# Performance work log

Hardware: AMD Instinct MI355X
Metric: run time of the kernel (lower is better)

Reference implementation:

```python
import jax, jax.numpy as jnp
from jax import lax
import numpy as np

INPUT_DIM = 64
AUX_DIM = 32
HIDDEN = [512, 512]
OUTPUT_DIM = 128
BATCH = 64
SEQ = 512


def _lstm_params(key, in_dim, hidden):
    # PyTorch nn.LSTM init: U(-1/sqrt(H), 1/sqrt(H)); gate order i,f,g,o
    k = 1.0 / np.sqrt(hidden)
    ks = jax.random.split(key, 4)
    W_ih = jax.random.uniform(ks[0], (4 * hidden, in_dim), jnp.float32, -k, k)
    W_hh = jax.random.uniform(ks[1], (4 * hidden, hidden), jnp.float32, -k, k)
    b_ih = jax.random.uniform(ks[2], (4 * hidden,), jnp.float32, -k, k)
    b_hh = jax.random.uniform(ks[3], (4 * hidden,), jnp.float32, -k, k)
    return W_ih, W_hh, b_ih, b_hh


def setup_inputs() -> dict:
    key = jax.random.key(0)
    k_x, k_aux, k_l0, k_l1, k_w, k_b = jax.random.split(key, 6)
    primary_input = jax.random.normal(k_x, (BATCH, SEQ, INPUT_DIM), jnp.float32)
    auxiliary_input = jax.random.normal(k_aux, (BATCH, AUX_DIM), jnp.float32)
    W_ih0, W_hh0, b_ih0, b_hh0 = _lstm_params(k_l0, INPUT_DIM + AUX_DIM, HIDDEN[0])
    W_ih1, W_hh1, b_ih1, b_hh1 = _lstm_params(k_l1, HIDDEN[0], HIDDEN[1])
    k_out = 1.0 / np.sqrt(HIDDEN[-1])
    W_out = jax.random.uniform(k_w, (OUTPUT_DIM, HIDDEN[-1]), jnp.float32, -k_out, k_out)
    b_out = jax.random.uniform(k_b, (OUTPUT_DIM,), jnp.float32, -k_out, k_out)
    return {
        "primary_input": primary_input, "auxiliary_input": auxiliary_input,
        "W_ih0": W_ih0, "W_hh0": W_hh0, "b_ih0": b_ih0, "b_hh0": b_hh0,
        "W_ih1": W_ih1, "W_hh1": W_hh1, "b_ih1": b_ih1, "b_hh1": b_hh1,
        "W_out": W_out, "b_out": b_out,
    }


def _lstm_layer(x, W_ih, W_hh, b_ih, b_hh):
    # x: [B, S, D] -> hidden sequence [B, S, H]; zero initial (h, c)
    B = x.shape[0]
    H = W_hh.shape[1]
    # Precompute input projection for all timesteps: [B, S, 4H]
    x_proj = jnp.einsum('bsd,gd->bsg', x, W_ih) + b_ih + b_hh

    def step(carry, xt):
        h, c = carry  # [B, H] each
        gates = xt + h @ W_hh.T  # [B, 4H]
        i, f, g, o = jnp.split(gates, 4, axis=-1)
        i = jax.nn.sigmoid(i)
        f = jax.nn.sigmoid(f)
        g = jnp.tanh(g)
        o = jax.nn.sigmoid(o)
        c = f * c + i * g
        h = o * jnp.tanh(c)
        return (h, c), h

    h0 = jnp.zeros((B, H), x.dtype)
    (_, _), hs = lax.scan(step, (h0, h0), jnp.swapaxes(x_proj, 0, 1))
    return jnp.swapaxes(hs, 0, 1)  # [B, S, H]


def reference(primary_input, auxiliary_input,
              W_ih0, W_hh0, b_ih0, b_hh0,
              W_ih1, W_hh1, b_ih1, b_hh1,
              W_out, b_out):
    S = primary_input.shape[1]
    aux = jnp.broadcast_to(auxiliary_input[:, None, :],
                           (auxiliary_input.shape[0], S, auxiliary_input.shape[1]))
    x = jnp.concatenate([primary_input, aux], axis=2)  # [B, S, input+aux]
    x = _lstm_layer(x, W_ih0, W_hh0, b_ih0, b_hh0)
    x = _lstm_layer(x, W_ih1, W_hh1, b_ih1, b_hh1)
    last = x[:, -1, :]  # [B, H]
    return last @ W_out.T + b_out  # [B, output_dim]
```

## Files before the change

### kernel.cpp

```cpp
#include <hip/hip_runtime.h>

#define BATCH 64
#define SEQ   512
#define HID   512
#define DPRIM 64
#define DAUX  32
#define CT    16
#define NCHUNK 32
#define NBAT  32
#define WP    520
#define XPI   104
#define PST   33

#define WS_HB0HI  0u
#define WS_HB0LO  131072u
#define WS_HB1HI  262144u
#define WS_HB1LO  393216u
#define WS_SLOT0  524288u
#define WS_SLOT1  526336u
#define WS_GDONE  528384u
#define WS_XPD    530432u
#define WS_STATE_END 532480u
#define WS_PHH0HI 532480u
#define WS_PHH0LO 2629632u
#define WS_PHH1HI 4726784u
#define WS_PHH1LO 6823936u
#define WS_PIH1HI 8921088u
#define WS_PIH1LO 11018240u
#define WS_PIH0HI 13115392u
#define WS_PIH0LO 13508608u
#define WS_BSUM0  13901824u
#define WS_BSUM1  13910016u
#define WS_WOT    13918208u
#define WS_HIST   14180352u
#define WS_XP0    18374656u
#define WS_XP1    26763264u

typedef short s16x8 __attribute__((ext_vector_type(8)));
typedef float f32x4 __attribute__((ext_vector_type(4)));
typedef unsigned long long u64t;
typedef unsigned int u32t;
typedef unsigned short u16t;

__device__ __forceinline__ float sigm(float x)  { return 1.f / (1.f + __expf(-x)); }
__device__ __forceinline__ float tanh_f(float x){ return 1.f - 2.f / (__expf(2.f * x) + 1.f); }
__device__ __forceinline__ u16t f2b(float f) {
    u32t u = __float_as_uint(f);
    u += 0x7fffu + ((u >> 16) & 1u);
    return (u16t)(u >> 16);
}
__device__ __forceinline__ void split2(float f, u16t* hi, u16t* lo) {
    u16t h = f2b(f);
    float r = f - __uint_as_float((u32t)h << 16);
    *hi = h; *lo = f2b(r);
}
__device__ __forceinline__ u64t ld_coh64(const u64t* p) {
    return __hip_atomic_load(p, __ATOMIC_RELAXED, __HIP_MEMORY_SCOPE_AGENT);
}
__device__ __forceinline__ float ld_cohf(const float* p) {
    return __hip_atomic_load(p, __ATOMIC_RELAXED, __HIP_MEMORY_SCOPE_AGENT);
}
__device__ __forceinline__ void st_coh32(u32t* p, u32t v) {
    __hip_atomic_store(p, v, __ATOMIC_RELAXED, __HIP_MEMORY_SCOPE_AGENT);
}
__device__ __forceinline__ void st_cohf(float* p, float v) {
    __hip_atomic_store(p, v, __ATOMIC_RELAXED, __HIP_MEMORY_SCOPE_AGENT);
}
__device__ __forceinline__ int ld_slot(const int* p) {
    return __hip_atomic_load(p, __ATOMIC_RELAXED, __HIP_MEMORY_SCOPE_AGENT);
}
__device__ __forceinline__ void st_slot(int* p, int v) {
    __hip_atomic_store(p, v, __ATOMIC_RELAXED, __HIP_MEMORY_SCOPE_AGENT);
}
#define MFMA16(a,b,c) __builtin_amdgcn_mfma_f32_16x16x32_bf16(a,b,c,0,0,0)

__device__ __forceinline__ void stage_w(const u16t* ph, const u16t* pl,
                                        u16t* dh, u16t* dl, int u0, int tid) {
    int rl = tid >> 4, j = tid & 15;
    int grow = (rl >> 3) * HID + u0 + (rl & 7);
    const u64t* sh = (const u64t*)(ph + (size_t)grow * HID);
    const u64t* sl = (const u64t*)(pl + (size_t)grow * HID);
    u64t* th = (u64t*)(dh + (size_t)rl * WP);
    u64t* tl2 = (u64t*)(dl + (size_t)rl * WP);
#pragma unroll
    for (int q = 0; q < 8; ++q) { int s = q * 16 + j; th[s] = sh[s]; tl2[s] = sl[s]; }
}

__global__ void prep_kernel(const float* __restrict__ Wih0, const float* __restrict__ Whh0,
                            const float* __restrict__ bih0, const float* __restrict__ bhh0,
                            const float* __restrict__ Wih1, const float* __restrict__ Whh1,
                            const float* __restrict__ bih1, const float* __restrict__ bhh1,
                            const float* __restrict__ Wout, char* __restrict__ ws)
{
    int idx = blockIdx.x * 256 + threadIdx.x;
    u16t h, l;
    split2(Whh0[idx], &h, &l);
    ((u16t*)(ws + WS_PHH0HI))[idx] = h; ((u16t*)(ws + WS_PHH0LO))[idx] = l;
    split2(Whh1[idx], &h, &l);
    ((u16t*)(ws + WS_PHH1HI))[idx] = h; ((u16t*)(ws + WS_PHH1LO))[idx] = l;
    split2(Wih1[idx], &h, &l);
    ((u16t*)(ws + WS_PIH1HI))[idx] = h; ((u16t*)(ws + WS_PIH1LO))[idx] = l;
    if (idx < 2048 * 96) {
        split2(Wih0[idx], &h, &l);
        ((u16t*)(ws + WS_PIH0HI))[idx] = h; ((u16t*)(ws + WS_PIH0LO))[idx] = l;
    }
    if (idx < 2048) {
        ((float*)(ws + WS_BSUM0))[idx] = bih0[idx] + bhh0[idx];
        ((float*)(ws + WS_BSUM1))[idx] = bih1[idx] + bhh1[idx];
    }
    if (idx < 65536) {
        ((float*)(ws + WS_WOT))[idx] = Wout[(size_t)(idx & 127) * HID + (idx >> 7)];
    }
}

__device__ __forceinline__ void do_step(
    int t, int c, int tl, int tid, int wid, int col, int kg,
    int b0, int u0, int ug,
    u16t* Whi, u16t* Wlo, u16t* Hhi, u16t* Hlo, float* Ps, float* Cs,
    u16t* hbhi, u16t* hblo, int* slots_self,
    const float* xp_self, bool coh_xq, u32t* hist_ring)
{
    const int p = t & 1;
    float xq0 = 0.f, xq1 = 0.f, xq2 = 0.f, xq3 = 0.f;
    if (tid < 256) {
        int b = tid >> 3, u = tid & 7;
        const float* xr = xp_self + (size_t)(b * CT + tl) * 32;
        if (coh_xq) {
            xq0 = ld_cohf(xr + u);      xq1 = ld_cohf(xr + 8 + u);
            xq2 = ld_cohf(xr + 16 + u); xq3 = ld_cohf(xr + 24 + u);
        } else {
            xq0 = xr[u]; xq1 = xr[8 + u]; xq2 = xr[16 + u]; xq3 = xr[24 + u];
        }
    }
    if (tid < 64) {
        while (true) {
            int v = ld_slot(slots_self + tid * 4);
            if (__all(v >= t)) break;
            __builtin_amdgcn_s_sleep(1);
        }
    }
    __syncthreads();
    {
        int b = tid >> 4, j = tid & 15;
        const u64t* sh = (const u64t*)(hbhi + (size_t)((p ^ 1) * BATCH + b0 + b) * HID);
        const u64t* sl = (const u64t*)(hblo + (size_t)((p ^ 1) * BATCH + b0 + b) * HID);
        u64t* th = (u64t*)(Hhi + (size_t)b * WP);
        u64t* tl2 = (u64t*)(Hlo + (size_t)b * WP);
#pragma unroll
        for (int q = 0; q < 8; ++q) {
            int s = q * 16 + j;
            u64t vh = ld_coh64(sh + s);
            u64t vl = ld_coh64(sl + s);
            th[s] = vh; tl2[s] = vl;
        }
    }
    __syncthreads();
    if (wid < 4) {
        int rt = wid >> 1, bt = wid & 1;
        const u16t* wah = Whi + (size_t)(rt * 16 + col) * WP;
        const u16t* wal = Wlo + (size_t)(rt * 16 + col) * WP;
        const u16t* hbh = Hhi + (size_t)(bt * 16 + col) * WP;
        const u16t* hbl = Hlo + (size_t)(bt * 16 + col) * WP;
        f32x4 a0 = {0.f, 0.f, 0.f, 0.f}, a1 = {0.f, 0.f, 0.f, 0.f};
#pragma unroll
        for (int k2 = 0; k2 < 8; ++k2) {
            int ko0 = k2 * 64 + kg * 8;
            int ko1 = ko0 + 32;
            s16x8 ah0 = *(const s16x8*)(wah + ko0), al0 = *(const s16x8*)(wal + ko0);
            s16x8 bh0 = *(const s16x8*)(hbh + ko0), bl0 = *(const s16x8*)(hbl + ko0);
            s16x8 ah1 = *(const s16x8*)(wah + ko1), al1 = *(const s16x8*)(wal + ko1);
            s16x8 bh1 = *(const s16x8*)(hbh + ko1), bl1 = *(const s16x8*)(hbl + ko1);
            a0 = MFMA16(ah0, bh0, a0); a1 = MFMA16(ah1, bh1, a1);
            a0 = MFMA16(ah0, bl0, a0); a1 = MFMA16(ah1, bl1, a1);
            a0 = MFMA16(al0, bh0, a0); a1 = MFMA16(al1, bh1, a1);
        }
        a0 = a0 + a1;
#pragma unroll
        for (int j = 0; j < 4; ++j)
            Ps[(rt * 16 + kg * 4 + j) * PST + bt * 16 + col] = a0[j];
    }
    __syncthreads();
    if (tid < 256) {
        int b = tid >> 3, u = tid & 7;
        float gi = Ps[(u)      * PST + b] + xq0;
        float gf = Ps[(8 + u)  * PST + b] + xq1;
        float gg = Ps[(16 + u) * PST + b] + xq2;
        float go = Ps[(24 + u) * PST + b] + xq3;
        float si = sigm(gi), sf = sigm(gf), so = sigm(go);
        float tg = tanh_f(gg);
        float cN = sf * Cs[tid] + si * tg;
        Cs[tid] = cN;
        float hN = so * tanh_f(cN);
        u16t hi, lo; split2(hN, &hi, &lo);
        int e = (b0 + b) * HID + u0 + u;
        int ph = __shfl_xor((int)hi, 1);
        int pl = __shfl_xor((int)lo, 1);
        if ((u & 1) == 0) {
            st_coh32((u32t*)hbhi + (size_t)p * (BATCH * HID / 2) + (e >> 1),
                     (u32t)hi | ((u32t)ph << 16));
            st_coh32((u32t*)hblo + (size_t)p * (BATCH * HID / 2) + (e >> 1),
                     (u32t)lo | ((u32t)pl << 16));
        }
        if (hist_ring) {
            st_coh32(hist_ring + ((size_t)((c & 1) * BATCH + b0 + b) * CT + tl) * HID + u0 + u,
                     ((u32t)hi << 16) | (u32t)lo);
        }
    }
    __syncthreads();
    if (tid == 0) st_slot(slots_self + ug * 4, t + 1);
}

__global__ __launch_bounds__(512, 2)
void mega_kernel(const float* __restrict__ prim, const float* __restrict__ aux,
                 char* __restrict__ ws)
{
    __shared__ __align__(16) unsigned char smem[151808];
    u16t* Whi  = (u16t*)smem;
    u16t* Wlo  = (u16t*)(smem + 33280);
    u16t* Hhi  = (u16t*)(smem + 66560);
    u16t* Hlo  = (u16t*)(smem + 99840);
    u16t* XWhi = (u16t*)(smem + 133120);
    u16t* XWlo = (u16t*)(smem + 139776);
    float* Ps  = (float*)(smem + 146432);
    float* Cs  = (float*)(smem + 150656);
    float* Bs  = (float*)(smem + 151680);

    const int tid  = threadIdx.x;
    const int wgid = blockIdx.x;
    const int layer = wgid >> 7;
    const int lwg  = wgid & 127;
    const int bg   = (lwg >> 2) & 1;
    const int ug   = ((lwg >> 3) << 2) | (lwg & 3);
    const int b0   = bg * NBAT;
    const int u0   = ug * 8;
    const int lane = tid & 63;
    const int wid  = tid >> 6;
    const int col  = lane & 15;
    const int kg   = lane >> 4;

    u16t* hbhi = (u16t*)(ws + (layer ? WS_HB1HI : WS_HB0HI));
    u16t* hblo = (u16t*)(ws + (layer ? WS_HB1LO : WS_HB0LO));
    int* slots_self = (int*)(ws + (layer ? WS_SLOT1 : WS_SLOT0)) + bg * 256;
    int* slots_l0   = (int*)(ws + WS_SLOT0) + bg * 256;
    int* gdone      = (int*)(ws + WS_GDONE) + bg * 256;
    int* xpd        = (int*)(ws + WS_XPD)   + bg * 256;
    const float* bsum = (const float*)(ws + (layer ? WS_BSUM1 : WS_BSUM0));
    u32t* hist = (u32t*)(ws + WS_HIST);
    float* xpregion = (float*)(ws + (layer ? WS_XP1 : WS_XP0));
    float* xp_self = xpregion + (size_t)lwg * 16384;

    if (tid < 256) Cs[tid] = 0.f;
    if (tid < 32) {
        int grow = (tid >> 3) * HID + u0 + (tid & 7);
        Bs[tid] = bsum[grow];
    }
    if (layer == 0) {
        stage_w((u16t*)(ws + WS_PHH0HI), (u16t*)(ws + WS_PHH0LO), Whi, Wlo, u0, tid);
        for (int s = tid; s < 32 * 24; s += 512) {
            int rl = s / 24, sl = s % 24;
            int grow = (rl >> 3) * HID + u0 + (rl & 7);
            u64t v  = *((const u64t*)((u16t*)(ws + WS_PIH0HI) + (size_t)grow * 96) + sl);
            u64t v2 = *((const u64t*)((u16t*)(ws + WS_PIH0LO) + (size_t)grow * 96) + sl);
            *((u64t*)(XWhi + (size_t)rl * XPI) + sl) = v;
            *((u64t*)(XWlo + (size_t)rl * XPI) + sl) = v2;
        }
    }
    __syncthreads();

    if (layer == 0) {
        for (int c = 0; c < NCHUNK; ++c) {
            {
                f32x4 acc[4][2];
#pragma unroll
                for (int m4 = 0; m4 < 4; ++m4)
#pragma unroll
                    for (int nt = 0; nt < 2; ++nt)
                        acc[m4][nt] = (f32x4){0.f, 0.f, 0.f, 0.f};
#pragma unroll
                for (int kt = 0; kt < 3; ++kt) {
                    int k0 = kt * 32 + kg * 8;
                    s16x8 ah0 = *(const s16x8*)(XWhi + (size_t)(col) * XPI + k0);
                    s16x8 al0 = *(const s16x8*)(XWlo + (size_t)(col) * XPI + k0);
                    s16x8 ah1 = *(const s16x8*)(XWhi + (size_t)(16 + col) * XPI + k0);
                    s16x8 al1 = *(const s16x8*)(XWlo + (size_t)(16 + col) * XPI + k0);
#pragma unroll
                    for (int m4 = 0; m4 < 4; ++m4) {
                        int bb = wid * 4 + m4;
                        float xv[8];
                        if (kt < 2) {
                            const float* pr = prim + ((size_t)(b0 + bb) * SEQ + c * CT + col) * DPRIM + k0;
                            float4 v0 = *(const float4*)pr;
                            float4 v1 = *(const float4*)(pr + 4);
                            xv[0] = v0.x; xv[1] = v0.y; xv[2] = v0.z; xv[3] = v0.w;
                            xv[4] = v1.x; xv[5] = v1.y; xv[6] = v1.z; xv[7] = v1.w;
                        } else {
                            const float* ax = aux + (size_t)(b0 + bb) * DAUX + kg * 8;
                            float4 v0 = *(const float4*)ax;
                            float4 v1 = *(const float4*)(ax + 4);
                            xv[0] = v0.x; xv[1] = v0.y; xv[2] = v0.z; xv[3] = v0.w;
                            xv[4] = v1.x; xv[5] = v1.y; xv[6] = v1.z; xv[7] = v1.w;
                        }
                        u16t hh[8], ll[8];
#pragma unroll
                        for (int j = 0; j < 8; ++j) split2(xv[j], &hh[j], &ll[j]);
                        s16x8 bh, bl;
#pragma unroll
                        for (int j = 0; j < 8; ++j) { bh[j] = (short)hh[j]; bl[j] = (short)ll[j]; }
                        acc[m4][0] = MFMA16(ah0, bh, acc[m4][0]);
                        acc[m4][0] = MFMA16(ah0, bl, acc[m4][0]);
                        acc[m4][0] = MFMA16(al0, bh, acc[m4][0]);
                        acc[m4][1] = MFMA16(ah1, bh, acc[m4][1]);
                        acc[m4][1] = MFMA16(ah1, bl, acc[m4][1]);
                        acc[m4][1] = MFMA16(al1, bh, acc[m4][1]);
                    }
                }
#pragma unroll
                for (int m4 = 0; m4 < 4; ++m4) {
                    int m = (wid * 4 + m4) * 16 + col;
#pragma unroll
                    for (int nt = 0; nt < 2; ++nt)
#pragma unroll
                        for (int j = 0; j < 4; ++j) {
                            int gr = nt * 16 + kg * 4 + j;
                            xp_self[(size_t)m * 32 + gr] = acc[m4][nt][j] + Bs[gr];
                        }
                }
            }
            if (c >= 2) {
                if (tid < 64) {
                    while (true) {
                        int v = ld_slot(gdone + tid * 4);
                        if (__all(v >= c - 1)) break;
                        __builtin_amdgcn_s_sleep(1);
                    }
                }
            }
            __syncthreads();
            for (int tl = 0; tl < CT; ++tl)
                do_step(c * CT + tl, c, tl, tid, wid, col, kg, b0, u0, ug,
                        Whi, Wlo, Hhi, Hlo, Ps, Cs, hbhi, hblo, slots_self,
                        xp_self, false, hist);
        }
    } else {
        u16t* Bthi = Whi;
        u16t* Btlo = Hhi;
        const int gm = ug >> 3, gn = ug & 7;
        for (int c = 0; c < NCHUNK; ++c) {
            if (tid < 64) {
                while (true) {
                    int v = ld_slot(slots_l0 + tid * 4);
                    if (__all(v >= (c + 1) * CT)) break;
                    __builtin_amdgcn_s_sleep(1);
                }
            }
            __syncthreads();
            {
                int i = tid >> 3, j = tid & 7;
                int m = gm * 64 + i;
                int gb = b0 + (m >> 4), tl2 = m & 15;
                const u64t* src = (const u64t*)(hist + ((size_t)((c & 1) * BATCH + gb) * CT + tl2) * HID);
                u64t* dh = (u64t*)(Bthi + (size_t)i * WP);
                u64t* dl = (u64t*)(Btlo + (size_t)i * WP);
#pragma unroll
                for (int q = 0; q < 16; ++q) {
                    int g = q * 8 + j;
                    u64t w0 = ld_coh64(src + g * 2);
                    u64t w1 = ld_coh64(src + g * 2 + 1);
                    u32t e0 = (u32t)w0, e1 = (u32t)(w0 >> 32);
                    u32t e2 = (u32t)w1, e3 = (u32t)(w1 >> 32);
                    dh[g] = (u64t)(e0 >> 16) | ((u64t)(e1 >> 16) << 16) |
                            ((u64t)(e2 >> 16) << 32) | ((u64t)(e3 >> 16) << 48);
                    dl[g] = (u64t)(e0 & 0xffffu) | ((u64t)(e1 & 0xffffu) << 16) |
                            ((u64t)(e2 & 0xffffu) << 32) | ((u64t)(e3 & 0xffffu) << 48);
                }
            }
            __syncthreads();
            if (tid == 0) st_slot(gdone + ug * 4, c + 1);
            {
                const u16t* pih = (const u16t*)(ws + WS_PIH1HI);
                const u16t* pil = (const u16t*)(ws + WS_PIH1LO);
                int Rb0 = gn * 256 + (wid * 2) * 16 + col;
                int Rb1 = Rb0 + 16;
                int g0 = ((Rb0 >> 3) & 3) * HID + (Rb0 >> 5) * 8 + (Rb0 & 7);
                int g1 = ((Rb1 >> 3) & 3) * HID + (Rb1 >> 5) * 8 + (Rb1 & 7);
                const u16t* a0h = pih + (size_t)g0 * HID;
                const u16t* a0l = pil + (size_t)g0 * HID;
                const u16t* a1h = pih + (size_t)g1 * HID;
                const u16t* a1l = pil + (size_t)g1 * HID;
                float biasv[2][4];
#pragma unroll
                for (int nt = 0; nt < 2; ++nt)
#pragma unroll
                    for (int j = 0; j < 4; ++j) {
                        int R = gn * 256 + (wid * 2 + nt) * 16 + kg * 4 + j;
                        biasv[nt][j] = bsum[((R >> 3) & 3) * HID + (R >> 5) * 8 + (R & 7)];
                    }
                f32x4 acc[4][2];
#pragma unroll
                for (int mt = 0; mt < 4; ++mt)
#pragma unroll
                    for (int nt = 0; nt < 2; ++nt)
                        acc[mt][nt] = (f32x4){0.f, 0.f, 0.f, 0.f};
                for (int kt = 0; kt < 16; ++kt) {
                    int k0 = kt * 32 + kg * 8;
                    s16x8 ah0 = *(const s16x8*)(a0h + k0), al0 = *(const s16x8*)(a0l + k0);
                    s16x8 ah1 = *(const s16x8*)(a1h + k0), al1 = *(const s16x8*)(a1l + k0);
#pragma unroll
                    for (int mt = 0; mt < 4; ++mt) {
                        const u16t* bth = Bthi + (size_t)(mt * 16 + col) * WP;
                        const u16t* btl = Btlo + (size_t)(mt * 16 + col) * WP;
                        s16x8 bh = *(const s16x8*)(bth + k0), bl = *(const s16x8*)(btl + k0);
                        acc[mt][0] = MFMA16(ah0, bh, acc[mt][0]);
                        acc[mt][0] = MFMA16(ah0, bl, acc[mt][0]);
                        acc[mt][0] = MFMA16(al0, bh, acc[mt][0]);
                        acc[mt][1] = MFMA16(ah1, bh, acc[mt][1]);
                        acc[mt][1] = MFMA16(ah1, bl, acc[mt][1]);
                        acc[mt][1] = MFMA16(al1, bh, acc[mt][1]);
                    }
                }
#pragma unroll
                for (int mt = 0; mt < 4; ++mt)
#pragma unroll
                    for (int nt = 0; nt < 2; ++nt)
#pragma unroll
                        for (int j = 0; j < 4; ++j) {
                            int m = gm * 64 + mt * 16 + col;
                            int R = gn * 256 + (wid * 2 + nt) * 16 + kg * 4 + j;
                            int ugt = R >> 5, rl = R & 31;
                            int lwgt = ((ugt >> 2) << 3) | (bg << 2) | (ugt & 3);
                            st_cohf(xpregion + (size_t)lwgt * 16384 + (size_t)m * 32 + rl,
                                    acc[mt][nt][j] + biasv[nt][j]);
                        }
            }
            __syncthreads();
            if (tid == 0) st_slot(xpd + ug * 4, c + 1);
            stage_w((u16t*)(ws + WS_PHH1HI), (u16t*)(ws + WS_PHH1LO), Whi, Wlo, u0, tid);
            if (tid < 64) {
                while (true) {
                    int v = ld_slot(xpd + tid * 4);
                    if (__all(v >= c + 1)) break;
                    __builtin_amdgcn_s_sleep(1);
                }
            }
            __syncthreads();
            for (int tl = 0; tl < CT; ++tl)
                do_step(c * CT + tl, c, tl, tid, wid, col, kg, b0, u0, ug,
                        Whi, Wlo, Hhi, Hlo, Ps, Cs, hbhi, hblo, slots_self,
                        xp_self, true, nullptr);
        }
    }
}

__global__ void outproj_kernel(const char* __restrict__ ws, const float* __restrict__ bout,
                               float* __restrict__ out)
{
    __shared__ float hs[HID];
    int b = blockIdx.x;
    const u16t* hh = (const u16t*)(ws + WS_HB1HI) + (size_t)(BATCH + b) * HID;
    const u16t* hl = (const u16t*)(ws + WS_HB1LO) + (size_t)(BATCH + b) * HID;
    for (int i = threadIdx.x; i < HID; i += 128)
        hs[i] = __uint_as_float((u32t)hh[i] << 16) + __uint_as_float((u32t)hl[i] << 16);
    __syncthreads();
    int o = threadIdx.x;
    const float* Wot = (const float*)(ws + WS_WOT);
    float acc = bout[o];
#pragma unroll 8
    for (int k = 0; k < HID; ++k) acc = fmaf(hs[k], Wot[k * 128 + o], acc);
    out[b * 128 + o] = acc;
}

extern "C" void kernel_launch(void* const* d_in, const int* in_sizes, int n_in,
                              void* d_out, int out_size, void* d_ws, size_t ws_size,
                              hipStream_t stream)
{
    (void)in_sizes; (void)n_in; (void)out_size; (void)ws_size;
    const float* prim = (const float*)d_in[0];
    const float* aux  = (const float*)d_in[1];
    const float* Wih0 = (const float*)d_in[2];
    const float* Whh0 = (const float*)d_in[3];
    const float* bih0 = (const float*)d_in[4];
    const float* bhh0 = (const float*)d_in[5];
    const float* Wih1 = (const float*)d_in[6];
    const float* Whh1 = (const float*)d_in[7];
    const float* bih1 = (const float*)d_in[8];
    const float* bhh1 = (const float*)d_in[9];
    const float* Wout = (const float*)d_in[10];
    const float* bout = (const float*)d_in[11];
    float* out = (float*)d_out;
    char* wsc  = (char*)d_ws;

    hipMemsetAsync(wsc, 0, WS_STATE_END, stream);
    prep_kernel<<<4096, 256, 0, stream>>>(Wih0, Whh0, bih0, bhh0,
                                          Wih1, Whh1, bih1, bhh1, Wout, wsc);

    void* margs[] = {(void*)&prim, (void*)&aux, (void*)&wsc};
    hipLaunchCooperativeKernel((void*)mega_kernel, dim3(256), dim3(512), margs, 0, stream);

    outproj_kernel<<<64, 128, 0, stream>>>(wsc, bout, out);
}
```

Before: 3.701 ms.

## Keep recurrent weights in registers and split K across all eight waves

The per-step recurrent matmul now uses all 8 waves, splitting K in half, instead of only 4. Each wave holds its W_hh fragments in registers for the whole chunk, and the previous hidden state is loaded straight from global memory into MFMA operands rather than staged through LDS. The aim is to cut two __syncthreads and the LDS staging from every serial timestep, and partial sums from the two K halves are added in the gate stage. Each wave now spin-waits only on the 32 slots it needs, and h and history stores are widened to 64-bit. The cost is higher register pressure and more polling traffic per wave.

```diff
diff --git a/kernel.cpp b/kernel.cpp
--- a/kernel.cpp
+++ b/kernel.cpp
@@ -38,6 +38,7 @@
 
 typedef short s16x8 __attribute__((ext_vector_type(8)));
 typedef float f32x4 __attribute__((ext_vector_type(4)));
+typedef unsigned long long u64x2 __attribute__((ext_vector_type(2)));
 typedef unsigned long long u64t;
 typedef unsigned int u32t;
 typedef unsigned short u16t;
@@ -54,13 +55,17 @@
     float r = f - __uint_as_float((u32t)h << 16);
     *hi = h; *lo = f2b(r);
 }
+__device__ __forceinline__ s16x8 mk_s16x8(u64t a, u64t b) {
+    u64x2 t; t.x = a; t.y = b;
+    return __builtin_bit_cast(s16x8, t);
+}
 __device__ __forceinline__ u64t ld_coh64(const u64t* p) {
     return __hip_atomic_load(p, __ATOMIC_RELAXED, __HIP_MEMORY_SCOPE_AGENT);
 }
 __device__ __forceinline__ float ld_cohf(const float* p) {
     return __hip_atomic_load(p, __ATOMIC_RELAXED, __HIP_MEMORY_SCOPE_AGENT);
 }
-__device__ __forceinline__ void st_coh32(u32t* p, u32t v) {
+__device__ __forceinline__ void st_coh64w(u64t* p, u64t v) {
     __hip_atomic_store(p, v, __ATOMIC_RELAXED, __HIP_MEMORY_SCOPE_AGENT);
 }
 __device__ __forceinline__ void st_cohf(float* p, float v) {
@@ -74,16 +79,19 @@
 }
 #define MFMA16(a,b,c) __builtin_amdgcn_mfma_f32_16x16x32_bf16(a,b,c,0,0,0)
 
-__device__ __forceinline__ void stage_w(const u16t* ph, const u16t* pl,
-                                        u16t* dh, u16t* dl, int u0, int tid) {
-    int rl = tid >> 4, j = tid & 15;
-    int grow = (rl >> 3) * HID + u0 + (rl & 7);
-    const u64t* sh = (const u64t*)(ph + (size_t)grow * HID);
-    const u64t* sl = (const u64t*)(pl + (size_t)grow * HID);
-    u64t* th = (u64t*)(dh + (size_t)rl * WP);
-    u64t* tl2 = (u64t*)(dl + (size_t)rl * WP);
-#pragma unroll
-    for (int q = 0; q < 8; ++q) { int s = q * 16 + j; th[s] = sh[s]; tl2[s] = sl[s]; }
+__device__ __forceinline__ void load_afrag(const u16t* ph, const u16t* pl,
+                                           int u0, int col, int kg, int rt, int kh,
+                                           s16x8* ah, s16x8* al) {
+    int r = rt * 16 + col;
+    int grow = (r >> 3) * HID + u0 + (r & 7);
+    const u16t* sh = ph + (size_t)grow * HID;
+    const u16t* sl = pl + (size_t)grow * HID;
+#pragma unroll
+    for (int k2 = 0; k2 < 8; ++k2) {
+        int ko = (kh * 8 + k2) * 32 + kg * 8;
+        ah[k2] = *(const s16x8*)(sh + ko);
+        al[k2] = *(const s16x8*)(sl + ko);
+    }
 }
 
 __global__ void prep_kernel(const float* __restrict__ Wih0, const float* __restrict__ Whh0,
@@ -114,9 +122,11 @@
 }
 
 __device__ __forceinline__ void do_step(
-    int t, int c, int tl, int tid, int wid, int col, int kg,
+    int t, int c, int tl, int tid, int col, int kg,
+    int rt, int bt, int kh,
     int b0, int u0, int ug,
-    u16t* Whi, u16t* Wlo, u16t* Hhi, u16t* Hlo, float* Ps, float* Cs,
+    const s16x8* ah, const s16x8* al,
+    float* Ps, float* Cs,
     u16t* hbhi, u16t* hblo, int* slots_self,
     const float* xp_self, bool coh_xq, u32t* hist_ring)
 {
@@ -132,78 +142,67 @@
             xq0 = xr[u]; xq1 = xr[8 + u]; xq2 = xr[16 + u]; xq3 = xr[24 + u];
         }
     }
-    if (tid < 64) {
+    {
+        int lane = tid & 63;
+        const int* sp = slots_self + (kh * 32 + (lane & 31)) * 4;
         while (true) {
-            int v = ld_slot(slots_self + tid * 4);
+            int v = (lane < 32) ? ld_slot(sp) : 0x7fffffff;
             if (__all(v >= t)) break;
             __builtin_amdgcn_s_sleep(1);
         }
     }
-    __syncthreads();
-    {
-        int b = tid >> 4, j = tid & 15;
-        const u64t* sh = (const u64t*)(hbhi + (size_t)((p ^ 1) * BATCH + b0 + b) * HID);
-        const u64t* sl = (const u64t*)(hblo + (size_t)((p ^ 1) * BATCH + b0 + b) * HID);
-        u64t* th = (u64t*)(Hhi + (size_t)b * WP);
-        u64t* tl2 = (u64t*)(Hlo + (size_t)b * WP);
-#pragma unroll
-        for (int q = 0; q < 8; ++q) {
-            int s = q * 16 + j;
-            u64t vh = ld_coh64(sh + s);
-            u64t vl = ld_coh64(sl + s);
-            th[s] = vh; tl2[s] = vl;
-        }
-    }
-    __syncthreads();
-    if (wid < 4) {
-        int rt = wid >> 1, bt = wid & 1;
-        const u16t* wah = Whi + (size_t)(rt * 16 + col) * WP;
-        const u16t* wal = Wlo + (size_t)(rt * 16 + col) * WP;
-        const u16t* hbh = Hhi + (size_t)(bt * 16 + col) * WP;
-        const u16t* hbl = Hlo + (size_t)(bt * 16 + col) * WP;
-        f32x4 a0 = {0.f, 0.f, 0.f, 0.f}, a1 = {0.f, 0.f, 0.f, 0.f};
-#pragma unroll
-        for (int k2 = 0; k2 < 8; ++k2) {
-            int ko0 = k2 * 64 + kg * 8;
-            int ko1 = ko0 + 32;
-            s16x8 ah0 = *(const s16x8*)(wah + ko0), al0 = *(const s16x8*)(wal + ko0);
-            s16x8 bh0 = *(const s16x8*)(hbh + ko0), bl0 = *(const s16x8*)(hbl + ko0);
-            s16x8 ah1 = *(const s16x8*)(wah + ko1), al1 = *(const s16x8*)(wal + ko1);
-            s16x8 bh1 = *(const s16x8*)(hbh + ko1), bl1 = *(const s16x8*)(hbl + ko1);
-            a0 = MFMA16(ah0, bh0, a0); a1 = MFMA16(ah1, bh1, a1);
-            a0 = MFMA16(ah0, bl0, a0); a1 = MFMA16(ah1, bl1, a1);
-            a0 = MFMA16(al0, bh0, a0); a1 = MFMA16(al1, bh1, a1);
-        }
-        a0 = a0 + a1;
-#pragma unroll
-        for (int j = 0; j < 4; ++j)
-            Ps[(rt * 16 + kg * 4 + j) * PST + bt * 16 + col] = a0[j];
-    }
+    asm volatile("" ::: "memory");
+    const size_t brow = (size_t)((p ^ 1) * BATCH + b0 + bt * 16 + col) * HID;
+    s16x8 bh[8], bl[8];
+#pragma unroll
+    for (int k2 = 0; k2 < 8; ++k2) {
+        int ko = (kh * 8 + k2) * 32 + kg * 8;
+        u64t h0 = ld_coh64((const u64t*)(hbhi + brow + ko));
+        u64t h1 = ld_coh64((const u64t*)(hbhi + brow + ko + 4));
+        u64t l0 = ld_coh64((const u64t*)(hblo + brow + ko));
+        u64t l1 = ld_coh64((const u64t*)(hblo + brow + ko + 4));
+        bh[k2] = mk_s16x8(h0, h1);
+        bl[k2] = mk_s16x8(l0, l1);
+    }
+    f32x4 a0 = {0.f, 0.f, 0.f, 0.f}, a1 = {0.f, 0.f, 0.f, 0.f};
+#pragma unroll
+    for (int k2 = 0; k2 < 8; ++k2) {
+        a0 = MFMA16(ah[k2], bh[k2], a0);
+        a1 = MFMA16(ah[k2], bl[k2], a1);
+        a0 = MFMA16(al[k2], bh[k2], a0);
+    }
+    a0 = a0 + a1;
+#pragma unroll
+    for (int j = 0; j < 4; ++j)
+        Ps[((kh << 5) + rt * 16 + kg * 4 + j) * PST + bt * 16 + col] = a0[j];
     __syncthreads();
     if (tid < 256) {
         int b = tid >> 3, u = tid & 7;
-        float gi = Ps[(u)      * PST + b] + xq0;
-        float gf = Ps[(8 + u)  * PST + b] + xq1;
-        float gg = Ps[(16 + u) * PST + b] + xq2;
-        float go = Ps[(24 + u) * PST + b] + xq3;
+        float gi = Ps[(u)      * PST + b] + Ps[(32 + u) * PST + b] + xq0;
+        float gf = Ps[(8 + u)  * PST + b] + Ps[(40 + u) * PST + b] + xq1;
+        float gg = Ps[(16 + u) * PST + b] + Ps[(48 + u) * PST + b] + xq2;
+        float go = Ps[(24 + u) * PST + b] + Ps[(56 + u) * PST + b] + xq3;
         float si = sigm(gi), sf = sigm(gf), so = sigm(go);
         float tg = tanh_f(gg);
         float cN = sf * Cs[tid] + si * tg;
         Cs[tid] = cN;
         float hN = so * tanh_f(cN);
         u16t hi, lo; split2(hN, &hi, &lo);
-        int e = (b0 + b) * HID + u0 + u;
-        int ph = __shfl_xor((int)hi, 1);
-        int pl = __shfl_xor((int)lo, 1);
-        if ((u & 1) == 0) {
-            st_coh32((u32t*)hbhi + (size_t)p * (BATCH * HID / 2) + (e >> 1),
-                     (u32t)hi | ((u32t)ph << 16));
-            st_coh32((u32t*)hblo + (size_t)p * (BATCH * HID / 2) + (e >> 1),
-                     (u32t)lo | ((u32t)pl << 16));
+        u32t wh = (u32t)hi | (((u32t)(u16t)__shfl_xor((int)hi, 1)) << 16);
+        u32t wl = (u32t)lo | (((u32t)(u16t)__shfl_xor((int)lo, 1)) << 16);
+        u64t qh = (u64t)wh | ((u64t)(u32t)__shfl_xor((int)wh, 2) << 32);
+        u64t ql = (u64t)wl | ((u64t)(u32t)__shfl_xor((int)wl, 2) << 32);
+        size_t e = ((size_t)p * BATCH + b0 + b) * HID + u0 + u;
+        if ((u & 3) == 0) {
+            st_coh64w((u64t*)hbhi + (e >> 2), qh);
+            st_coh64w((u64t*)hblo + (e >> 2), ql);
         }
         if (hist_ring) {
-            st_coh32(hist_ring + ((size_t)((c & 1) * BATCH + b0 + b) * CT + tl) * HID + u0 + u,
-                     ((u32t)hi << 16) | (u32t)lo);
+            u32t pk = ((u32t)hi << 16) | (u32t)lo;
+            u64t qp = (u64t)pk | ((u64t)(u32t)__shfl_xor((int)pk, 1) << 32);
+            if ((u & 1) == 0)
+                st_coh64w((u64t*)(hist_ring +
+                    ((size_t)((c & 1) * BATCH + b0 + b) * CT + tl) * HID + u0 + u), qp);
         }
     }
     __syncthreads();
@@ -214,16 +213,14 @@
 void mega_kernel(const float* __restrict__ prim, const float* __restrict__ aux,
                  char* __restrict__ ws)
 {
-    __shared__ __align__(16) unsigned char smem[151808];
-    u16t* Whi  = (u16t*)smem;
-    u16t* Wlo  = (u16t*)(smem + 33280);
-    u16t* Hhi  = (u16t*)(smem + 66560);
-    u16t* Hlo  = (u16t*)(smem + 99840);
+    __shared__ __align__(16) unsigned char smem[156032];
+    u16t* Bthi = (u16t*)smem;
+    u16t* Btlo = (u16t*)(smem + 66560);
     u16t* XWhi = (u16t*)(smem + 133120);
     u16t* XWlo = (u16t*)(smem + 139776);
     float* Ps  = (float*)(smem + 146432);
-    float* Cs  = (float*)(smem + 150656);
-    float* Bs  = (float*)(smem + 151680);
+    float* Cs  = (float*)(smem + 154880);
+    float* Bs  = (float*)(smem + 155904);
 
     const int tid  = threadIdx.x;
     const int wgid = blockIdx.x;
@@ -237,6 +234,9 @@
     const int wid  = tid >> 6;
     const int col  = lane & 15;
     const int kg   = lane >> 4;
+    const int rt   = (wid >> 1) & 1;
+    const int bt   = wid & 1;
+    const int kh   = wid >> 2;
 
     u16t* hbhi = (u16t*)(ws + (layer ? WS_HB1HI : WS_HB0HI));
     u16t* hblo = (u16t*)(ws + (layer ? WS_HB1LO : WS_HB0LO));
@@ -255,7 +255,6 @@
         Bs[tid] = bsum[grow];
     }
     if (layer == 0) {
-        stage_w((u16t*)(ws + WS_PHH0HI), (u16t*)(ws + WS_PHH0LO), Whi, Wlo, u0, tid);
         for (int s = tid; s < 32 * 24; s += 512) {
             int rl = s / 24, sl = s % 24;
             int grow = (rl >> 3) * HID + u0 + (rl & 7);
@@ -303,15 +302,15 @@
                         u16t hh[8], ll[8];
 #pragma unroll
                         for (int j = 0; j < 8; ++j) split2(xv[j], &hh[j], &ll[j]);
-                        s16x8 bh, bl;
-#pragma unroll
-                        for (int j = 0; j < 8; ++j) { bh[j] = (short)hh[j]; bl[j] = (short)ll[j]; }
-                        acc[m4][0] = MFMA16(ah0, bh, acc[m4][0]);
-                        acc[m4][0] = MFMA16(ah0, bl, acc[m4][0]);
-                        acc[m4][0] = MFMA16(al0, bh, acc[m4][0]);
-                        acc[m4][1] = MFMA16(ah1, bh, acc[m4][1]);
-                        acc[m4][1] = MFMA16(ah1, bl, acc[m4][1]);
-                        acc[m4][1] = MFMA16(al1, bh, acc[m4][1]);
+                        s16x8 bhv, blv;
+#pragma unroll
+                        for (int j = 0; j < 8; ++j) { bhv[j] = (short)hh[j]; blv[j] = (short)ll[j]; }
+                        acc[m4][0] = MFMA16(ah0, bhv, acc[m4][0]);
+                        acc[m4][0] = MFMA16(ah0, blv, acc[m4][0]);
+                        acc[m4][0] = MFMA16(al0, bhv, acc[m4][0]);
+                        acc[m4][1] = MFMA16(ah1, bhv, acc[m4][1]);
+                        acc[m4][1] = MFMA16(ah1, blv, acc[m4][1]);
+                        acc[m4][1] = MFMA16(al1, bhv, acc[m4][1]);
                     }
                 }
 #pragma unroll
@@ -326,6 +325,9 @@
                         }
                 }
             }
+            s16x8 ahf[8], alf[8];
+            load_afrag((const u16t*)(ws + WS_PHH0HI), (const u16t*)(ws + WS_PHH0LO),
+                       u0, col, kg, rt, kh, ahf, alf);
             if (c >= 2) {
                 if (tid < 64) {
                     while (true) {
@@ -337,13 +339,11 @@
             }
             __syncthreads();
             for (int tl = 0; tl < CT; ++tl)
-                do_step(c * CT + tl, c, tl, tid, wid, col, kg, b0, u0, ug,
-                        Whi, Wlo, Hhi, Hlo, Ps, Cs, hbhi, hblo, slots_self,
+                do_step(c * CT + tl, c, tl, tid, col, kg, rt, bt, kh, b0, u0, ug,
+                        ahf, alf, Ps, Cs, hbhi, hblo, slots_self,
                         xp_self, false, hist);
         }
     } else {
-        u16t* Bthi = Whi;
-        u16t* Btlo = Hhi;
         const int gm = ug >> 3, gn = ug & 7;
         for (int c = 0; c < NCHUNK; ++c) {
             if (tid < 64) {
@@ -409,13 +409,13 @@
                     for (int mt = 0; mt < 4; ++mt) {
                         const u16t* bth = Bthi + (size_t)(mt * 16 + col) * WP;
                         const u16t* btl = Btlo + (size_t)(mt * 16 + col) * WP;
-                        s16x8 bh = *(const s16x8*)(bth + k0), bl = *(const s16x8*)(btl + k0);
-                        acc[mt][0] = MFMA16(ah0, bh, acc[mt][0]);
-                        acc[mt][0] = MFMA16(ah0, bl, acc[mt][0]);
-                        acc[mt][0] = MFMA16(al0, bh, acc[mt][0]);
-                        acc[mt][1] = MFMA16(ah1, bh, acc[mt][1]);
-                        acc[mt][1] = MFMA16(ah1, bl, acc[mt][1]);
-                        acc[mt][1] = MFMA16(al1, bh, acc[mt][1]);
+                        s16x8 bhv = *(const s16x8*)(bth + k0), blv = *(const s16x8*)(btl + k0);
+                        acc[mt][0] = MFMA16(ah0, bhv, acc[mt][0]);
+                        acc[mt][0] = MFMA16(ah0, blv, acc[mt][0]);
+                        acc[mt][0] = MFMA16(al0, bhv, acc[mt][0]);
+                        acc[mt][1] = MFMA16(ah1, bhv, acc[mt][1]);
+                        acc[mt][1] = MFMA16(ah1, blv, acc[mt][1]);
+                        acc[mt][1] = MFMA16(al1, bhv, acc[mt][1]);
                     }
                 }
 #pragma unroll
@@ -434,7 +434,9 @@
             }
             __syncthreads();
             if (tid == 0) st_slot(xpd + ug * 4, c + 1);
-            stage_w((u16t*)(ws + WS_PHH1HI), (u16t*)(ws + WS_PHH1LO), Whi, Wlo, u0, tid);
+            s16x8 ahf[8], alf[8];
+            load_afrag((const u16t*)(ws + WS_PHH1HI), (const u16t*)(ws + WS_PHH1LO),
+                       u0, col, kg, rt, kh, ahf, alf);
             if (tid < 64) {
                 while (true) {
                     int v = ld_slot(xpd + tid * 4);
@@ -444,8 +446,8 @@
             }
             __syncthreads();
             for (int tl = 0; tl < CT; ++tl)
-                do_step(c * CT + tl, c, tl, tid, wid, col, kg, b0, u0, ug,
-                        Whi, Wlo, Hhi, Hlo, Ps, Cs, hbhi, hblo, slots_self,
+                do_step(c * CT + tl, c, tl, tid, col, kg, rt, bt, kh, b0, u0, ug,
+                        ahf, alf, Ps, Cs, hbhi, hblo, slots_self,
                         xp_self, true, nullptr);
         }
     }
```

New measurement: 6.500 ms. +75.6%, slower.
